# Optimization experiments

Hardware: AMD Instinct MI355X
Metric: run time of the kernel (lower is better)

## Reference

```python
import jax, jax.numpy as jnp
import numpy as np

B, D, H = 8, 14, 128          # trees, GCMN_DEPTH, HIDDEN_SIZE
N_LEAF = 2 ** (D - 1)          # leaves (= depth-1 nodes) per tree


def _build_tree():
    # level[d] = node ids at depth d within one tree
    level = [np.arange(N_LEAF, dtype=np.int32)]
    cur = N_LEAF
    for d in range(1, D + 1):
        cnt = N_LEAF >> (d - 1)
        level.append(np.arange(cur, cur + cnt, dtype=np.int32))
        cur += cnt
    npt = cur                                  # nodes per tree = 3n - 1
    offs = (np.arange(B, dtype=np.int32) * npt)[:, None]

    def batched(a):
        return (a[None, :] + offs).reshape(-1)

    src, dst, st = [], [], []
    # leaf block: depth-0 node -> its unique depth-1 node (edge_states = 0)
    src.append(batched(level[0]))
    dst.append(batched(level[1]))
    st.append(np.zeros(B * N_LEAF, np.float32))
    # depth d -> d+1 blocks: left children first, then right children
    for d in range(1, D):
        ch, pa = level[d], level[d + 1]
        left, right = ch[0::2], ch[1::2]
        src.append(np.concatenate([batched(left), batched(right)]))
        dst.append(np.concatenate([batched(pa), batched(pa)]))
        m = B * len(ch)
        st.append(np.concatenate([np.zeros(m // 2, np.float32), np.ones(m // 2, np.float32)]))
    return (np.concatenate(src), np.concatenate(dst), np.concatenate(st), B * npt)


def _dense(key, fin, fout):
    return jax.random.normal(key, (fin, fout), jnp.float32) / np.sqrt(fin)


def setup_inputs() -> dict:
    key = jax.random.key(0)
    esrc, edst, estates, n_nodes = _build_tree()
    ks = jax.random.split(key, 24)
    inp = {
        "x": jax.random.normal(ks[0], (n_nodes, H), jnp.float32),
        "edge_src": jnp.asarray(esrc),
        "edge_dst": jnp.asarray(edst),
        "edge_states": jnp.asarray(estates),
        "edge_features": jax.random.normal(ks[1], (B * N_LEAF, H), jnp.float32),
        "gcmn_depth": D,
    }
    specs = {"nem": 2 * H, "mg": 2 * H, "mr": H + 1}  # WideMLP input widths
    i = 2
    for name, fin in specs.items():
        dims = [(fin, H), (H, H), (H, H)]
        for j, (a, b) in enumerate(dims):
            inp[f"{name}_w{j}"] = _dense(ks[i], a, b); i += 1
            inp[f"{name}_b{j}"] = jnp.zeros((b,), jnp.float32)
    return inp


def _mlp3(h, w0, b0, w1, b1, w2, b2):
    # WideMLP(in, hidden, out, HIDDEN_LAYERS=2): two ReLU hidden layers + linear out
    h = jax.nn.relu(h @ w0 + b0)
    h = jax.nn.relu(h @ w1 + b1)
    return h @ w2 + b2


def reference(x, edge_src, edge_dst, edge_states, edge_features,
              nem_w0, nem_b0, nem_w1, nem_b1, nem_w2, nem_b2,
              mg_w0, mg_b0, mg_w1, mg_b1, mg_w2, mg_b2,
              mr_w0, mr_b0, mr_w1, mr_b1, mr_w2, mr_b2,
              gcmn_depth):
    Dn = int(gcmn_depth)
    nL = edge_features.shape[0]
    N = x.shape[0]
    # static offsets of the per-depth edge blocks (edges are depth-sorted)
    block_off = [0]
    off = nL
    for d in range(1, Dn):
        block_off.append(off)
        off += nL >> (d - 1)

    # ---- forward_up ----
    start_feat = x[edge_src[:nL]]                       # depth-0 node features
    merged = _mlp3(jnp.concatenate([start_feat, edge_features], axis=1),
                   nem_w0, nem_b0, nem_w1, nem_b1, nem_w2, nem_b2)
    x = x.at[edge_dst[:nL]].set(merged)                 # write depth-1 nodes
    for d in range(1, Dn):
        s = block_off[d]
        m = nL >> (d - 1)
        half = m // 2
        left = x[edge_src[s:s + half]]                  # edge_states == 0
        right = x[edge_src[s + half:s + m]]             # edge_states == 1
        par = edge_dst[s + half:s + m]
        x = x.at[par].set(_mlp3(jnp.concatenate([left, right], axis=1),
                                mg_w0, mg_b0, mg_w1, mg_b1, mg_w2, mg_b2))

    # ---- forward_down ----
    for depth in range(Dn, 0, -1):
        if depth == 1:
            s, m = 0, nL
        else:
            s = block_off[depth - 1]
            m = nL >> (depth - 2)
        src = edge_src[s:s + m]
        dst = edge_dst[s:s + m]
        st = edge_states[s:s + m]
        top = x[dst]
        bottom = x[src]
        merged = _mlp3(jnp.concatenate([top, st[:, None]], axis=1),
                       mr_w0, mr_b0, mr_w1, mr_b1, mr_w2, mr_b2)
        agg = jax.ops.segment_sum(merged, src, num_segments=N)  # scatter_sum
        x = x.at[src].set(agg[src] + bottom)
    return x
```

## Files before the change

### kernel.cpp

```cpp
#include <hip/hip_runtime.h>
#include <cstdint>
#include <cstddef>

typedef __attribute__((ext_vector_type(8))) short bf16x8;
typedef __attribute__((ext_vector_type(4))) float f32x4;

#define LO_OFF 184320

__device__ __forceinline__ unsigned short f2bf(float f) {
  union { float f; unsigned u; } c; c.f = f;
  unsigned u = c.u + 0x7fffu + ((c.u >> 16) & 1u);
  return (unsigned short)(u >> 16);
}
__device__ __forceinline__ float bf2f(unsigned short h) {
  union { unsigned u; float f; } c; c.u = ((unsigned)h) << 16;
  return c.f;
}

struct PrepP {
  const float* w[9];
  unsigned short* out;
};

__global__ __launch_bounds__(256) void prep_kernel(PrepP pp) {
  int gid = blockIdx.x * 256 + threadIdx.x;
  if (gid >= LO_OFF) return;
  const int Ks[9]  = {256,128,128, 256,128,128, 129,128,128};
  const int szs[9] = {32768,16384,16384, 32768,16384,16384, 20480,16384,16384};
  const int KCs[9] = {8,4,4, 8,4,4, 5,4,4};
  int m = 0, off = gid;
  while (m < 8 && off >= szs[m]) { off -= szs[m]; ++m; }
  int j    = off & 7;
  int t    = off >> 3;
  int lane = t & 63;
  int fc   = t >> 6;
  int KC   = KCs[m];
  int kc   = fc % KC;
  int nt   = fc / KC;
  int n = nt * 16 + (lane & 15);
  int k = kc * 32 + (lane >> 4) * 8 + j;
  float v = 0.f;
  if (k < Ks[m]) v = pp.w[m][(size_t)k * 128 + n];
  unsigned short hi = f2bf(v);
  unsigned short lo = f2bf(v - bf2f(hi));
  pp.out[gid] = hi;
  pp.out[LO_OFF + gid] = lo;
}

struct FP {
  const float* srcA;
  const float* srcB;
  const float* addbase;
  const int* esrc;
  const int* edst;
  const float* est;
  const unsigned short* w0;
  const unsigned short* w1;
  const unsigned short* w2;
  const float* b0;
  const float* b1;
  const float* b2;
  float* out;
  int s, half, rows;
};

template<int KC>
__device__ __forceinline__ void mfma_layer_to_h(
    char* AH, char* AL, int lane, int wrow0,
    const unsigned short* w, const float* bias) {
  bf16x8 ah[KC], al[KC];
  int arow = wrow0 + (lane & 15);
  int aswz = (arow & 7) << 4;
  #pragma unroll
  for (int kc = 0; kc < KC; ++kc) {
    int byt = (kc * 64 + (lane >> 4) * 16) ^ aswz;
    ah[kc] = *(const bf16x8*)(AH + arow * 512 + byt);
    al[kc] = *(const bf16x8*)(AL + arow * 512 + byt);
  }
  #pragma unroll
  for (int nt = 0; nt < 8; ++nt) {
    float bv = bias[nt * 16 + (lane & 15)];
    f32x4 acc = {bv, bv, bv, bv};
    #pragma unroll
    for (int kc = 0; kc < KC; ++kc) {
      const char* wb = (const char*)(w + (size_t)(nt * KC + kc) * 512) + lane * 16;
      bf16x8 bh = *(const bf16x8*)(wb);
      bf16x8 bl = *(const bf16x8*)(wb + (size_t)LO_OFF * 2);
      acc = __builtin_amdgcn_mfma_f32_16x16x32_bf16(ah[kc], bh, acc, 0, 0, 0);
      acc = __builtin_amdgcn_mfma_f32_16x16x32_bf16(ah[kc], bl, acc, 0, 0, 0);
      acc = __builtin_amdgcn_mfma_f32_16x16x32_bf16(al[kc], bh, acc, 0, 0, 0);
    }
    #pragma unroll
    for (int r = 0; r < 4; ++r) {
      float v = fmaxf(acc[r], 0.f);
      int row = wrow0 + (lane >> 4) * 4 + r;
      int cb = (nt * 32 + (lane & 15) * 2) ^ ((row & 7) << 4);
      unsigned short hv = f2bf(v);
      *(unsigned short*)(AH + row * 512 + cb) = hv;
      *(unsigned short*)(AL + row * 512 + cb) = f2bf(v - bf2f(hv));
    }
  }
}

__device__ __forceinline__ void stage_write(char* AH, char* AL, int row, int byt, float4 v) {
  unsigned short h0 = f2bf(v.x), h1 = f2bf(v.y), h2 = f2bf(v.z), h3 = f2bf(v.w);
  uint2 hw, lw;
  hw.x = (unsigned)h0 | ((unsigned)h1 << 16);
  hw.y = (unsigned)h2 | ((unsigned)h3 << 16);
  lw.x = (unsigned)f2bf(v.x - bf2f(h0)) | ((unsigned)f2bf(v.y - bf2f(h1)) << 16);
  lw.y = (unsigned)f2bf(v.z - bf2f(h2)) | ((unsigned)f2bf(v.w - bf2f(h3)) << 16);
  *(uint2*)(AH + row * 512 + byt) = hw;
  *(uint2*)(AL + row * 512 + byt) = lw;
}

template<int MODE>
__global__ __launch_bounds__(256) void fused_mlp(FP p) {
  __shared__ char AH[64 * 512];
  __shared__ char AL[64 * 512];
  const int tid = threadIdx.x;
  const int wid = tid >> 6;
  const int lane = tid & 63;
  const int tbase = blockIdx.x * 64;
  const int wrow0 = wid * 16;

  if (MODE != 2) {
    #pragma unroll
    for (int it = 0; it < 16; ++it) {
      int row = wrow0 + it;
      int rg = tbase + row;
      int f4 = lane;
      float4 v = {0.f, 0.f, 0.f, 0.f};
      if (rg < p.rows) {
        if (MODE == 0) {
          if (f4 < 32) { int node = p.esrc[rg]; v = *(const float4*)(p.srcA + (size_t)node * 128 + f4 * 4); }
          else         { v = *(const float4*)(p.srcB + (size_t)rg * 128 + (f4 - 32) * 4); }
        } else {
          if (f4 < 32) { int node = p.esrc[p.s + rg];          v = *(const float4*)(p.srcA + (size_t)node * 128 + f4 * 4); }
          else         { int node = p.esrc[p.s + p.half + rg]; v = *(const float4*)(p.srcA + (size_t)node * 128 + (f4 - 32) * 4); }
        }
      }
      int byt = (f4 * 8) ^ ((row & 7) << 4);
      stage_write(AH, AL, row, byt, v);
    }
  } else {
    #pragma unroll
    for (int it = 0; it < 8; ++it) {
      int li = it * 64 + lane;
      int rl = li >> 5;
      int f4 = li & 31;
      int row = wrow0 + rl;
      int rg = tbase + row;
      float4 v = {0.f, 0.f, 0.f, 0.f};
      if (rg < p.rows) { int node = p.edst[p.s + rg]; v = *(const float4*)(p.srcA + (size_t)node * 128 + f4 * 4); }
      int byt = (f4 * 8) ^ ((row & 7) << 4);
      stage_write(AH, AL, row, byt, v);
    }
    {
      int rl = lane >> 2;
      int ci = lane & 3;
      int row = wrow0 + rl;
      int rg = tbase + row;
      float sv = (rg < p.rows && ci == 0) ? p.est[p.s + rg] : 0.f;
      uint4 hz = {0u, 0u, 0u, 0u};
      uint4 lz = {0u, 0u, 0u, 0u};
      hz.x = (unsigned)f2bf(sv);
      int byt = (256 + ci * 16) ^ ((row & 7) << 4);
      *(uint4*)(AH + row * 512 + byt) = hz;
      *(uint4*)(AL + row * 512 + byt) = lz;
    }
  }
  __syncthreads();

  constexpr int KC0 = (MODE == 2) ? 5 : 8;
  mfma_layer_to_h<KC0>(AH, AL, lane, wrow0, p.w0, p.b0);
  __syncthreads();
  mfma_layer_to_h<4>(AH, AL, lane, wrow0, p.w1, p.b1);
  __syncthreads();

  {
    bf16x8 ah[4], al[4];
    int arow = wrow0 + (lane & 15);
    int aswz = (arow & 7) << 4;
    #pragma unroll
    for (int kc = 0; kc < 4; ++kc) {
      int byt = (kc * 64 + (lane >> 4) * 16) ^ aswz;
      ah[kc] = *(const bf16x8*)(AH + arow * 512 + byt);
      al[kc] = *(const bf16x8*)(AL + arow * 512 + byt);
    }
    int nodes[4]; bool vld[4];
    #pragma unroll
    for (int r = 0; r < 4; ++r) {
      int rg = tbase + wrow0 + (lane >> 4) * 4 + r;
      vld[r] = rg < p.rows;
      int e = 0;
      if (vld[r]) {
        if (MODE == 0)      e = p.edst[rg];
        else if (MODE == 1) e = p.edst[p.s + rg];
        else                e = p.esrc[p.s + rg];
      }
      nodes[r] = e;
    }
    #pragma unroll
    for (int nt = 0; nt < 8; ++nt) {
      float bv = p.b2[nt * 16 + (lane & 15)];
      f32x4 acc = {bv, bv, bv, bv};
      #pragma unroll
      for (int kc = 0; kc < 4; ++kc) {
        const char* wb = (const char*)(p.w2 + (size_t)(nt * 4 + kc) * 512) + lane * 16;
        bf16x8 bh = *(const bf16x8*)(wb);
        bf16x8 bl = *(const bf16x8*)(wb + (size_t)LO_OFF * 2);
        acc = __builtin_amdgcn_mfma_f32_16x16x32_bf16(ah[kc], bh, acc, 0, 0, 0);
        acc = __builtin_amdgcn_mfma_f32_16x16x32_bf16(ah[kc], bl, acc, 0, 0, 0);
        acc = __builtin_amdgcn_mfma_f32_16x16x32_bf16(al[kc], bh, acc, 0, 0, 0);
      }
      int col = nt * 16 + (lane & 15);
      #pragma unroll
      for (int r = 0; r < 4; ++r) {
        if (vld[r]) {
          float v = acc[r];
          if (MODE == 2) v += p.addbase[(size_t)nodes[r] * 128 + col];
          p.out[(size_t)nodes[r] * 128 + col] = v;
        }
      }
    }
  }
}

extern "C" void kernel_launch(void* const* d_in, const int* in_sizes, int n_in,
                              void* d_out, int out_size, void* d_ws, size_t ws_size,
                              hipStream_t stream) {
  const float* xin  = (const float*)d_in[0];
  const int*   esrc = (const int*)d_in[1];
  const int*   edst = (const int*)d_in[2];
  const float* est  = (const float*)d_in[3];
  const float* ef   = (const float*)d_in[4];
  unsigned short* wsb = (unsigned short*)d_ws;
  float* xw = (float*)d_out;

  PrepP pp;
  const int widx[9] = {6, 8, 10, 12, 14, 16, 18, 20, 22};
  for (int i = 0; i < 9; ++i) pp.w[i] = (const float*)d_in[widx[i]];
  pp.out = wsb;
  prep_kernel<<<dim3(720), dim3(256), 0, stream>>>(pp);

  int blk[14], off[14];
  blk[0] = 65536; off[0] = 0;
  for (int d = 1; d <= 13; ++d) { blk[d] = 65536 >> (d - 1); off[d] = off[d - 1] + blk[d - 1]; }

  auto fill = [&](FP& p, int s, int half, int rows, const float* addb,
                  int w0o, int w1o, int w2o, int b0i, int b1i, int b2i) {
    p.addbase = addb;
    p.esrc = esrc; p.edst = edst; p.est = est;
    p.w0 = wsb + w0o; p.w1 = wsb + w1o; p.w2 = wsb + w2o;
    p.b0 = (const float*)d_in[b0i]; p.b1 = (const float*)d_in[b1i]; p.b2 = (const float*)d_in[b2i];
    p.out = xw;
    p.s = s; p.half = half; p.rows = rows;
  };

  {
    FP p; p.srcA = xin; p.srcB = ef;
    fill(p, 0, 0, 65536, nullptr, 0, 32768, 49152, 7, 9, 11);
    fused_mlp<0><<<dim3(1024), dim3(256), 0, stream>>>(p);
  }
  for (int d = 1; d <= 13; ++d) {
    FP p; p.srcA = xw; p.srcB = xw;
    int rows = blk[d] / 2;
    fill(p, off[d], rows, rows, nullptr, 65536, 98304, 114688, 13, 15, 17);
    fused_mlp<1><<<dim3((rows + 63) / 64), dim3(256), 0, stream>>>(p);
  }
  for (int bi = 13; bi >= 0; --bi) {
    FP p; p.srcA = xw; p.srcB = xw;
    int rows = blk[bi];
    const float* addb = (bi == 0) ? xin : xw;
    fill(p, off[bi], 0, rows, addb, 131072, 151552, 167936, 19, 21, 23);
    fused_mlp<2><<<dim3((rows + 63) / 64), dim3(256), 0, stream>>>(p);
  }
}
```

Baseline: 1.036 ms.

## Fuse small tree levels into persistent kernel with grid barriers; shrink tiles to 16 rows

The small levels (up-pass depths 5-13 and down-pass levels 13-6) now run inside one persistent 128-block kernel that separates levels with an atomic-counter grid barrier, replacing many tiny launches. Tiles shrink from 64 to 16 rows per block, and the 4 waves split the output columns instead of the rows, which gives more blocks for the small levels and a smaller shared-memory footprint. The goal is to remove per-launch overhead and tail underutilisation on the serial level chain. In exchange, each block rereads weights for only 16 rows, the large levels get more blocks, and the spin barrier adds latency and depends on all 128 blocks being resident at once.

```diff
diff --git a/kernel.cpp b/kernel.cpp
--- a/kernel.cpp
+++ b/kernel.cpp
@@ -4,22 +4,31 @@
 
 typedef __attribute__((ext_vector_type(8))) short bf16x8;
 typedef __attribute__((ext_vector_type(4))) float f32x4;
+typedef unsigned short u16;
 
 #define LO_OFF 184320
-
-__device__ __forceinline__ unsigned short f2bf(float f) {
+#define MFMA16(a,b,c) __builtin_amdgcn_mfma_f32_16x16x32_bf16((a),(b),(c),0,0,0)
+
+__device__ __forceinline__ u16 f2bf(float f) {
   union { float f; unsigned u; } c; c.f = f;
   unsigned u = c.u + 0x7fffu + ((c.u >> 16) & 1u);
-  return (unsigned short)(u >> 16);
-}
-__device__ __forceinline__ float bf2f(unsigned short h) {
+  return (u16)(u >> 16);
+}
+__device__ __forceinline__ float bf2f(u16 h) {
   union { unsigned u; float f; } c; c.u = ((unsigned)h) << 16;
   return c.f;
 }
+__device__ __forceinline__ void split4(float4 v, uint2& hw, uint2& lw) {
+  u16 h0 = f2bf(v.x), h1 = f2bf(v.y), h2 = f2bf(v.z), h3 = f2bf(v.w);
+  hw.x = (unsigned)h0 | ((unsigned)h1 << 16);
+  hw.y = (unsigned)h2 | ((unsigned)h3 << 16);
+  lw.x = (unsigned)f2bf(v.x - bf2f(h0)) | ((unsigned)f2bf(v.y - bf2f(h1)) << 16);
+  lw.y = (unsigned)f2bf(v.z - bf2f(h2)) | ((unsigned)f2bf(v.w - bf2f(h3)) << 16);
+}
 
 struct PrepP {
   const float* w[9];
-  unsigned short* out;
+  u16* out;
 };
 
 __global__ __launch_bounds__(256) void prep_kernel(PrepP pp) {
@@ -41,188 +50,225 @@
   int k = kc * 32 + (lane >> 4) * 8 + j;
   float v = 0.f;
   if (k < Ks[m]) v = pp.w[m][(size_t)k * 128 + n];
-  unsigned short hi = f2bf(v);
-  unsigned short lo = f2bf(v - bf2f(hi));
+  u16 hi = f2bf(v);
+  u16 lo = f2bf(v - bf2f(hi));
   pp.out[gid] = hi;
   pp.out[LO_OFF + gid] = lo;
 }
 
-struct FP {
-  const float* srcA;
-  const float* srcB;
-  const float* addbase;
-  const int* esrc;
-  const int* edst;
-  const float* est;
-  const unsigned short* w0;
-  const unsigned short* w1;
-  const unsigned short* w2;
-  const float* b0;
-  const float* b1;
-  const float* b2;
+struct LP {
+  const float* srcA; const float* srcB; const float* addb;
+  const int* esrc; const int* edst; const float* est;
+  const u16 *w0, *w1, *w2;
+  const float *b0, *b1, *b2;
   float* out;
   int s, half, rows;
 };
 
-template<int KC>
-__device__ __forceinline__ void mfma_layer_to_h(
-    char* AH, char* AL, int lane, int wrow0,
-    const unsigned short* w, const float* bias) {
-  bf16x8 ah[KC], al[KC];
-  int arow = wrow0 + (lane & 15);
-  int aswz = (arow & 7) << 4;
+template<int KC, int LDA>
+__device__ __forceinline__ void layer_mid(const u16* AH, const u16* AL, u16* OH, u16* OL,
+                                          int lane, int wv, const u16* wgt, const float* bias) {
+  const int arow = lane & 15;
+  const int g = lane >> 4;
+  const int aswz = (arow & 7) << 4;
+  const char* ahb = (const char*)AH + arow * LDA;
+  const char* alb = (const char*)AL + arow * LDA;
+  const int nt0 = wv * 2;
+  float bv0 = bias[nt0 * 16 + arow];
+  float bv1 = bias[nt0 * 16 + 16 + arow];
+  f32x4 acc0 = {bv0, bv0, bv0, bv0};
+  f32x4 acc1 = {bv1, bv1, bv1, bv1};
   #pragma unroll
   for (int kc = 0; kc < KC; ++kc) {
-    int byt = (kc * 64 + (lane >> 4) * 16) ^ aswz;
-    ah[kc] = *(const bf16x8*)(AH + arow * 512 + byt);
-    al[kc] = *(const bf16x8*)(AL + arow * 512 + byt);
-  }
-  #pragma unroll
-  for (int nt = 0; nt < 8; ++nt) {
-    float bv = bias[nt * 16 + (lane & 15)];
-    f32x4 acc = {bv, bv, bv, bv};
-    #pragma unroll
-    for (int kc = 0; kc < KC; ++kc) {
-      const char* wb = (const char*)(w + (size_t)(nt * KC + kc) * 512) + lane * 16;
-      bf16x8 bh = *(const bf16x8*)(wb);
-      bf16x8 bl = *(const bf16x8*)(wb + (size_t)LO_OFF * 2);
-      acc = __builtin_amdgcn_mfma_f32_16x16x32_bf16(ah[kc], bh, acc, 0, 0, 0);
-      acc = __builtin_amdgcn_mfma_f32_16x16x32_bf16(ah[kc], bl, acc, 0, 0, 0);
-      acc = __builtin_amdgcn_mfma_f32_16x16x32_bf16(al[kc], bh, acc, 0, 0, 0);
+    int byt = (kc * 64 + g * 16) ^ aswz;
+    bf16x8 ah = *(const bf16x8*)(ahb + byt);
+    bf16x8 al = *(const bf16x8*)(alb + byt);
+    const u16* wb0 = wgt + (size_t)(nt0 * KC + kc) * 512 + lane * 8;
+    const u16* wb1 = wb0 + (size_t)KC * 512;
+    bf16x8 bh0 = *(const bf16x8*)wb0;
+    bf16x8 bl0 = *(const bf16x8*)(wb0 + LO_OFF);
+    bf16x8 bh1 = *(const bf16x8*)wb1;
+    bf16x8 bl1 = *(const bf16x8*)(wb1 + LO_OFF);
+    acc0 = MFMA16(ah, bh0, acc0); acc1 = MFMA16(ah, bh1, acc1);
+    acc0 = MFMA16(ah, bl0, acc0); acc1 = MFMA16(ah, bl1, acc1);
+    acc0 = MFMA16(al, bh0, acc0); acc1 = MFMA16(al, bh1, acc1);
+  }
+  #pragma unroll
+  for (int r = 0; r < 4; ++r) {
+    int row = g * 4 + r;
+    int oswz = (row & 7) << 4;
+    char* oh = (char*)OH + row * 256;
+    char* ol = (char*)OL + row * 256;
+    float v0 = fmaxf(acc0[r], 0.f);
+    float v1 = fmaxf(acc1[r], 0.f);
+    int c0 = ((nt0 * 16 + arow) * 2) ^ oswz;
+    int c1 = ((nt0 * 16 + 16 + arow) * 2) ^ oswz;
+    u16 h0 = f2bf(v0), h1 = f2bf(v1);
+    *(u16*)(oh + c0) = h0; *(u16*)(ol + c0) = f2bf(v0 - bf2f(h0));
+    *(u16*)(oh + c1) = h1; *(u16*)(ol + c1) = f2bf(v1 - bf2f(h1));
+  }
+}
+
+template<int MODE>
+__device__ __forceinline__ void layer_out(const u16* AH, const u16* AL,
+                                          int lane, int wv, const LP& p, int tbase) {
+  const int arow = lane & 15;
+  const int g = lane >> 4;
+  const int aswz = (arow & 7) << 4;
+  const char* ahb = (const char*)AH + arow * 256;
+  const char* alb = (const char*)AL + arow * 256;
+  const int nt0 = wv * 2;
+  float bv0 = p.b2[nt0 * 16 + arow];
+  float bv1 = p.b2[nt0 * 16 + 16 + arow];
+  f32x4 acc0 = {bv0, bv0, bv0, bv0};
+  f32x4 acc1 = {bv1, bv1, bv1, bv1};
+
+  int nodes[4]; bool vld[4];
+  #pragma unroll
+  for (int r = 0; r < 4; ++r) {
+    int rg = tbase + g * 4 + r;
+    vld[r] = rg < p.rows;
+    int e = 0;
+    if (vld[r]) e = (MODE == 2) ? p.esrc[p.s + rg]
+                 : ((MODE == 0) ? p.edst[rg] : p.edst[p.s + rg]);
+    nodes[r] = e;
+  }
+  #pragma unroll
+  for (int kc = 0; kc < 4; ++kc) {
+    int byt = (kc * 64 + g * 16) ^ aswz;
+    bf16x8 ah = *(const bf16x8*)(ahb + byt);
+    bf16x8 al = *(const bf16x8*)(alb + byt);
+    const u16* wb0 = p.w2 + (size_t)(nt0 * 4 + kc) * 512 + lane * 8;
+    const u16* wb1 = wb0 + (size_t)4 * 512;
+    bf16x8 bh0 = *(const bf16x8*)wb0;
+    bf16x8 bl0 = *(const bf16x8*)(wb0 + LO_OFF);
+    bf16x8 bh1 = *(const bf16x8*)wb1;
+    bf16x8 bl1 = *(const bf16x8*)(wb1 + LO_OFF);
+    acc0 = MFMA16(ah, bh0, acc0); acc1 = MFMA16(ah, bh1, acc1);
+    acc0 = MFMA16(ah, bl0, acc0); acc1 = MFMA16(ah, bl1, acc1);
+    acc0 = MFMA16(al, bh0, acc0); acc1 = MFMA16(al, bh1, acc1);
+  }
+  int col0 = nt0 * 16 + arow, col1 = col0 + 16;
+  #pragma unroll
+  for (int r = 0; r < 4; ++r) {
+    if (vld[r]) {
+      float v0 = acc0[r], v1 = acc1[r];
+      size_t b = (size_t)nodes[r] * 128;
+      if (MODE == 2) { v0 += p.addb[b + col0]; v1 += p.addb[b + col1]; }
+      p.out[b + col0] = v0;
+      p.out[b + col1] = v1;
     }
-    #pragma unroll
-    for (int r = 0; r < 4; ++r) {
-      float v = fmaxf(acc[r], 0.f);
-      int row = wrow0 + (lane >> 4) * 4 + r;
-      int cb = (nt * 32 + (lane & 15) * 2) ^ ((row & 7) << 4);
-      unsigned short hv = f2bf(v);
-      *(unsigned short*)(AH + row * 512 + cb) = hv;
-      *(unsigned short*)(AL + row * 512 + cb) = f2bf(v - bf2f(hv));
+  }
+}
+
+template<int MODE>
+__device__ __forceinline__ void mlp_tile(u16* SH, u16* SL, u16* HH, u16* HL,
+                                         const LP& p, int tbase) {
+  const int tid = threadIdx.x;
+  const int lane = tid & 63;
+  const int wv = tid >> 6;
+  {
+    int row = tid >> 4, q = tid & 15;
+    int rg = tbase + row;
+    int swz = (row & 7) << 4;
+    char* sh = (char*)SH + row * 512;
+    char* sl = (char*)SL + row * 512;
+    bool ok = rg < p.rows;
+    if (MODE != 2) {
+      const float* pL = nullptr; const float* pR = nullptr;
+      if (ok) {
+        if (MODE == 0) { pL = p.srcA + (size_t)p.esrc[rg] * 128; pR = p.srcB + (size_t)rg * 128; }
+        else           { pL = p.srcA + (size_t)p.esrc[p.s + rg] * 128;
+                         pR = p.srcA + (size_t)p.esrc[p.s + p.half + rg] * 128; }
+      }
+      #pragma unroll
+      for (int i = 0; i < 4; ++i) {
+        int f4 = q * 4 + i;
+        float4 v = {0.f, 0.f, 0.f, 0.f};
+        if (ok) v = (f4 < 32) ? *(const float4*)(pL + f4 * 4) : *(const float4*)(pR + (f4 - 32) * 4);
+        uint2 hw, lw; split4(v, hw, lw);
+        int byt = (f4 * 8) ^ swz;
+        *(uint2*)(sh + byt) = hw; *(uint2*)(sl + byt) = lw;
+      }
+    } else {
+      const float* pT = ok ? p.srcA + (size_t)p.edst[p.s + rg] * 128 : nullptr;
+      #pragma unroll
+      for (int i = 0; i < 2; ++i) {
+        int f4 = q * 2 + i;
+        float4 v = {0.f, 0.f, 0.f, 0.f};
+        if (ok) v = *(const float4*)(pT + f4 * 4);
+        uint2 hw, lw; split4(v, hw, lw);
+        int byt = (f4 * 8) ^ swz;
+        *(uint2*)(sh + byt) = hw; *(uint2*)(sl + byt) = lw;
+      }
+      if (q < 4) {
+        float sv = (q == 0 && ok) ? p.est[p.s + rg] : 0.f;
+        uint4 hz = {0u, 0u, 0u, 0u}, lz = {0u, 0u, 0u, 0u};
+        hz.x = (unsigned)f2bf(sv);
+        int byt = (256 + q * 16) ^ swz;
+        *(uint4*)(sh + byt) = hz;
+        *(uint4*)(sl + byt) = lz;
+      }
     }
   }
-}
-
-__device__ __forceinline__ void stage_write(char* AH, char* AL, int row, int byt, float4 v) {
-  unsigned short h0 = f2bf(v.x), h1 = f2bf(v.y), h2 = f2bf(v.z), h3 = f2bf(v.w);
-  uint2 hw, lw;
-  hw.x = (unsigned)h0 | ((unsigned)h1 << 16);
-  hw.y = (unsigned)h2 | ((unsigned)h3 << 16);
-  lw.x = (unsigned)f2bf(v.x - bf2f(h0)) | ((unsigned)f2bf(v.y - bf2f(h1)) << 16);
-  lw.y = (unsigned)f2bf(v.z - bf2f(h2)) | ((unsigned)f2bf(v.w - bf2f(h3)) << 16);
-  *(uint2*)(AH + row * 512 + byt) = hw;
-  *(uint2*)(AL + row * 512 + byt) = lw;
+  __syncthreads();
+  layer_mid<(MODE == 2 ? 5 : 8), 512>(SH, SL, HH, HL, lane, wv, p.w0, p.b0);
+  __syncthreads();
+  layer_mid<4, 256>(HH, HL, SH, SL, lane, wv, p.w1, p.b1);
+  __syncthreads();
+  layer_out<MODE>(SH, SL, lane, wv, p, tbase);
 }
 
 template<int MODE>
-__global__ __launch_bounds__(256) void fused_mlp(FP p) {
-  __shared__ char AH[64 * 512];
-  __shared__ char AL[64 * 512];
-  const int tid = threadIdx.x;
-  const int wid = tid >> 6;
-  const int lane = tid & 63;
-  const int tbase = blockIdx.x * 64;
-  const int wrow0 = wid * 16;
-
-  if (MODE != 2) {
-    #pragma unroll
-    for (int it = 0; it < 16; ++it) {
-      int row = wrow0 + it;
-      int rg = tbase + row;
-      int f4 = lane;
-      float4 v = {0.f, 0.f, 0.f, 0.f};
-      if (rg < p.rows) {
-        if (MODE == 0) {
-          if (f4 < 32) { int node = p.esrc[rg]; v = *(const float4*)(p.srcA + (size_t)node * 128 + f4 * 4); }
-          else         { v = *(const float4*)(p.srcB + (size_t)rg * 128 + (f4 - 32) * 4); }
-        } else {
-          if (f4 < 32) { int node = p.esrc[p.s + rg];          v = *(const float4*)(p.srcA + (size_t)node * 128 + f4 * 4); }
-          else         { int node = p.esrc[p.s + p.half + rg]; v = *(const float4*)(p.srcA + (size_t)node * 128 + (f4 - 32) * 4); }
-        }
-      }
-      int byt = (f4 * 8) ^ ((row & 7) << 4);
-      stage_write(AH, AL, row, byt, v);
+__global__ __launch_bounds__(256) void level_kernel(LP p) {
+  __shared__ u16 SH[16 * 256];
+  __shared__ u16 SL[16 * 256];
+  __shared__ u16 HH[16 * 128];
+  __shared__ u16 HL[16 * 128];
+  mlp_tile<MODE>(SH, SL, HH, HL, p, blockIdx.x * 16);
+}
+
+struct GP {
+  const int* esrc; const int* edst; const float* est;
+  float* xw;
+  const u16 *gw0, *gw1, *gw2; const float *gb0, *gb1, *gb2;
+  const u16 *rw0, *rw1, *rw2; const float *rb0, *rb1, *rb2;
+  unsigned* cnt;
+  int nlev;
+  int mode[17]; int s[17]; int rows[17];
+};
+
+__global__ __launch_bounds__(256) void fused_kernel(GP g) {
+  __shared__ u16 SH[16 * 256];
+  __shared__ u16 SL[16 * 256];
+  __shared__ u16 HH[16 * 128];
+  __shared__ u16 HL[16 * 128];
+  const unsigned nb = gridDim.x;
+  for (int li = 0; li < g.nlev; ++li) {
+    int rows = g.rows[li];
+    int tbase = blockIdx.x * 16;
+    if (tbase < rows) {
+      LP p;
+      p.esrc = g.esrc; p.edst = g.edst; p.est = g.est;
+      p.srcA = g.xw; p.srcB = g.xw; p.addb = g.xw; p.out = g.xw;
+      p.s = g.s[li]; p.half = rows; p.rows = rows;
+      if (g.mode[li] == 1) {
+        p.w0 = g.gw0; p.w1 = g.gw1; p.w2 = g.gw2; p.b0 = g.gb0; p.b1 = g.gb1; p.b2 = g.gb2;
+        mlp_tile<1>(SH, SL, HH, HL, p, tbase);
+      } else {
+        p.w0 = g.rw0; p.w1 = g.rw1; p.w2 = g.rw2; p.b0 = g.rb0; p.b1 = g.rb1; p.b2 = g.rb2;
+        mlp_tile<2>(SH, SL, HH, HL, p, tbase);
+      }
     }
-  } else {
-    #pragma unroll
-    for (int it = 0; it < 8; ++it) {
-      int li = it * 64 + lane;
-      int rl = li >> 5;
-      int f4 = li & 31;
-      int row = wrow0 + rl;
-      int rg = tbase + row;
-      float4 v = {0.f, 0.f, 0.f, 0.f};
-      if (rg < p.rows) { int node = p.edst[p.s + rg]; v = *(const float4*)(p.srcA + (size_t)node * 128 + f4 * 4); }
-      int byt = (f4 * 8) ^ ((row & 7) << 4);
-      stage_write(AH, AL, row, byt, v);
+    __syncthreads();
+    if (threadIdx.x == 0) {
+      __threadfence();
+      __hip_atomic_fetch_add(g.cnt + li, 1u, __ATOMIC_ACQ_REL, __HIP_MEMORY_SCOPE_AGENT);
+      while (__hip_atomic_load(g.cnt + li, __ATOMIC_ACQUIRE, __HIP_MEMORY_SCOPE_AGENT) < nb) {
+        __builtin_amdgcn_s_sleep(2);
+      }
     }
-    {
-      int rl = lane >> 2;
-      int ci = lane & 3;
-      int row = wrow0 + rl;
-      int rg = tbase + row;
-      float sv = (rg < p.rows && ci == 0) ? p.est[p.s + rg] : 0.f;
-      uint4 hz = {0u, 0u, 0u, 0u};
-      uint4 lz = {0u, 0u, 0u, 0u};
-      hz.x = (unsigned)f2bf(sv);
-      int byt = (256 + ci * 16) ^ ((row & 7) << 4);
-      *(uint4*)(AH + row * 512 + byt) = hz;
-      *(uint4*)(AL + row * 512 + byt) = lz;
-    }
-  }
-  __syncthreads();
-
-  constexpr int KC0 = (MODE == 2) ? 5 : 8;
-  mfma_layer_to_h<KC0>(AH, AL, lane, wrow0, p.w0, p.b0);
-  __syncthreads();
-  mfma_layer_to_h<4>(AH, AL, lane, wrow0, p.w1, p.b1);
-  __syncthreads();
-
-  {
-    bf16x8 ah[4], al[4];
-    int arow = wrow0 + (lane & 15);
-    int aswz = (arow & 7) << 4;
-    #pragma unroll
-    for (int kc = 0; kc < 4; ++kc) {
-      int byt = (kc * 64 + (lane >> 4) * 16) ^ aswz;
-      ah[kc] = *(const bf16x8*)(AH + arow * 512 + byt);
-      al[kc] = *(const bf16x8*)(AL + arow * 512 + byt);
-    }
-    int nodes[4]; bool vld[4];
-    #pragma unroll
-    for (int r = 0; r < 4; ++r) {
-      int rg = tbase + wrow0 + (lane >> 4) * 4 + r;
-      vld[r] = rg < p.rows;
-      int e = 0;
-      if (vld[r]) {
-        if (MODE == 0)      e = p.edst[rg];
-        else if (MODE == 1) e = p.edst[p.s + rg];
-        else                e = p.esrc[p.s + rg];
-      }
-      nodes[r] = e;
-    }
-    #pragma unroll
-    for (int nt = 0; nt < 8; ++nt) {
-      float bv = p.b2[nt * 16 + (lane & 15)];
-      f32x4 acc = {bv, bv, bv, bv};
-      #pragma unroll
-      for (int kc = 0; kc < 4; ++kc) {
-        const char* wb = (const char*)(p.w2 + (size_t)(nt * 4 + kc) * 512) + lane * 16;
-        bf16x8 bh = *(const bf16x8*)(wb);
-        bf16x8 bl = *(const bf16x8*)(wb + (size_t)LO_OFF * 2);
-        acc = __builtin_amdgcn_mfma_f32_16x16x32_bf16(ah[kc], bh, acc, 0, 0, 0);
-        acc = __builtin_amdgcn_mfma_f32_16x16x32_bf16(ah[kc], bl, acc, 0, 0, 0);
-        acc = __builtin_amdgcn_mfma_f32_16x16x32_bf16(al[kc], bh, acc, 0, 0, 0);
-      }
-      int col = nt * 16 + (lane & 15);
-      #pragma unroll
-      for (int r = 0; r < 4; ++r) {
-        if (vld[r]) {
-          float v = acc[r];
-          if (MODE == 2) v += p.addbase[(size_t)nodes[r] * 128 + col];
-          p.out[(size_t)nodes[r] * 128 + col] = v;
-        }
-      }
-    }
+    __syncthreads();
   }
 }
 
@@ -234,45 +280,62 @@
   const int*   edst = (const int*)d_in[2];
   const float* est  = (const float*)d_in[3];
   const float* ef   = (const float*)d_in[4];
-  unsigned short* wsb = (unsigned short*)d_ws;
+  u16* wsb = (u16*)d_ws;
   float* xw = (float*)d_out;
+  unsigned* cnt = (unsigned*)((char*)d_ws + 737280);
 
   PrepP pp;
   const int widx[9] = {6, 8, 10, 12, 14, 16, 18, 20, 22};
   for (int i = 0; i < 9; ++i) pp.w[i] = (const float*)d_in[widx[i]];
   pp.out = wsb;
   prep_kernel<<<dim3(720), dim3(256), 0, stream>>>(pp);
+  hipMemsetAsync(cnt, 0, 128, stream);
 
   int blk[14], off[14];
   blk[0] = 65536; off[0] = 0;
   for (int d = 1; d <= 13; ++d) { blk[d] = 65536 >> (d - 1); off[d] = off[d - 1] + blk[d - 1]; }
 
-  auto fill = [&](FP& p, int s, int half, int rows, const float* addb,
-                  int w0o, int w1o, int w2o, int b0i, int b1i, int b2i) {
-    p.addbase = addb;
-    p.esrc = esrc; p.edst = edst; p.est = est;
-    p.w0 = wsb + w0o; p.w1 = wsb + w1o; p.w2 = wsb + w2o;
-    p.b0 = (const float*)d_in[b0i]; p.b1 = (const float*)d_in[b1i]; p.b2 = (const float*)d_in[b2i];
-    p.out = xw;
-    p.s = s; p.half = half; p.rows = rows;
+  auto base = [&](LP& p) {
+    p.esrc = esrc; p.edst = edst; p.est = est; p.out = xw;
+    p.srcA = xw; p.srcB = xw; p.addb = xw;
   };
 
   {
-    FP p; p.srcA = xin; p.srcB = ef;
-    fill(p, 0, 0, 65536, nullptr, 0, 32768, 49152, 7, 9, 11);
-    fused_mlp<0><<<dim3(1024), dim3(256), 0, stream>>>(p);
-  }
-  for (int d = 1; d <= 13; ++d) {
-    FP p; p.srcA = xw; p.srcB = xw;
+    LP p; base(p);
+    p.srcA = xin; p.srcB = ef;
+    p.w0 = wsb + 0; p.w1 = wsb + 32768; p.w2 = wsb + 49152;
+    p.b0 = (const float*)d_in[7]; p.b1 = (const float*)d_in[9]; p.b2 = (const float*)d_in[11];
+    p.s = 0; p.half = 0; p.rows = 65536;
+    level_kernel<0><<<dim3(4096), dim3(256), 0, stream>>>(p);
+  }
+  for (int d = 1; d <= 4; ++d) {
+    LP p; base(p);
     int rows = blk[d] / 2;
-    fill(p, off[d], rows, rows, nullptr, 65536, 98304, 114688, 13, 15, 17);
-    fused_mlp<1><<<dim3((rows + 63) / 64), dim3(256), 0, stream>>>(p);
-  }
-  for (int bi = 13; bi >= 0; --bi) {
-    FP p; p.srcA = xw; p.srcB = xw;
+    p.w0 = wsb + 65536; p.w1 = wsb + 98304; p.w2 = wsb + 114688;
+    p.b0 = (const float*)d_in[13]; p.b1 = (const float*)d_in[15]; p.b2 = (const float*)d_in[17];
+    p.s = off[d]; p.half = rows; p.rows = rows;
+    level_kernel<1><<<dim3((rows + 15) / 16), dim3(256), 0, stream>>>(p);
+  }
+  {
+    GP g;
+    g.esrc = esrc; g.edst = edst; g.est = est; g.xw = xw; g.cnt = cnt;
+    g.gw0 = wsb + 65536; g.gw1 = wsb + 98304; g.gw2 = wsb + 114688;
+    g.gb0 = (const float*)d_in[13]; g.gb1 = (const float*)d_in[15]; g.gb2 = (const float*)d_in[17];
+    g.rw0 = wsb + 131072; g.rw1 = wsb + 151552; g.rw2 = wsb + 167936;
+    g.rb0 = (const float*)d_in[19]; g.rb1 = (const float*)d_in[21]; g.rb2 = (const float*)d_in[23];
+    int li = 0;
+    for (int d = 5; d <= 13; ++d) { g.mode[li] = 1; g.s[li] = off[d]; g.rows[li] = blk[d] / 2; ++li; }
+    for (int bi = 13; bi >= 6; --bi) { g.mode[li] = 2; g.s[li] = off[bi]; g.rows[li] = blk[bi]; ++li; }
+    g.nlev = li;
+    fused_kernel<<<dim3(128), dim3(256), 0, stream>>>(g);
+  }
+  for (int bi = 5; bi >= 0; --bi) {
+    LP p; base(p);
     int rows = blk[bi];
-    const float* addb = (bi == 0) ? xin : xw;
-    fill(p, off[bi], 0, rows, addb, 131072, 151552, 167936, 19, 21, 23);
-    fused_mlp<2><<<dim3((rows + 63) / 64), dim3(256), 0, stream>>>(p);
-  }
-}
+    p.addb = (bi == 0) ? xin : xw;
+    p.w0 = wsb + 131072; p.w1 = wsb + 151552; p.w2 = wsb + 167936;
+    p.b0 = (const float*)d_in[19]; p.b1 = (const float*)d_in[21]; p.b2 = (const float*)d_in[23];
+    p.s = off[bi]; p.half = 0; p.rows = rows;
+    level_kernel<2><<<dim3((rows + 15) / 16), dim3(256), 0, stream>>>(p);
+  }
+}
```

Result: faster. 982.3 us (-5.1%).

## Fuse small tree levels into one per-tree kernel and use per-wave tiles

Applied to the files above, without the earlier changes.

Levels 5–13 of the up pass and 13–6 of the down pass now run in one persistent kernel with one block per tree, synchronising levels with block barriers instead of separate kernel launches. The MLP tile is restructured so each wave owns its 16-row LDS tile, staging inputs in 128-column halves and keeping accumulators in registers, so there are no block-wide barriers. LDS drops to 32KB with launch_bounds(256,3) for higher occupancy. The fused kernel uses only 8 blocks, so parallelism on those levels is limited, and correctness depends on nodes of different trees never mixing, which the per-tree indexing assumes.

```diff
diff --git a/kernel.cpp b/kernel.cpp
--- a/kernel.cpp
+++ b/kernel.cpp
@@ -3,23 +3,37 @@
 #include <cstddef>
 
 typedef __attribute__((ext_vector_type(8))) short bf16x8;
+typedef bf16x8 __attribute__((may_alias)) bf16x8_a;
 typedef __attribute__((ext_vector_type(4))) float f32x4;
+typedef unsigned short u16;
+typedef u16 __attribute__((may_alias)) u16_a;
+typedef uint2 __attribute__((may_alias)) uint2_a;
+typedef uint4 __attribute__((may_alias)) uint4_a;
 
 #define LO_OFF 184320
-
-__device__ __forceinline__ unsigned short f2bf(float f) {
+#define MFMA16(a,b,c) __builtin_amdgcn_mfma_f32_16x16x32_bf16((a),(b),(c),0,0,0)
+#define LDS_FENCE() asm volatile("" ::: "memory")
+
+__device__ __forceinline__ u16 f2bf(float f) {
   union { float f; unsigned u; } c; c.f = f;
   unsigned u = c.u + 0x7fffu + ((c.u >> 16) & 1u);
-  return (unsigned short)(u >> 16);
-}
-__device__ __forceinline__ float bf2f(unsigned short h) {
+  return (u16)(u >> 16);
+}
+__device__ __forceinline__ float bf2f(u16 h) {
   union { unsigned u; float f; } c; c.u = ((unsigned)h) << 16;
   return c.f;
 }
+__device__ __forceinline__ void split4(float4 v, uint2& hw, uint2& lw) {
+  u16 h0 = f2bf(v.x), h1 = f2bf(v.y), h2 = f2bf(v.z), h3 = f2bf(v.w);
+  hw.x = (unsigned)h0 | ((unsigned)h1 << 16);
+  hw.y = (unsigned)h2 | ((unsigned)h3 << 16);
+  lw.x = (unsigned)f2bf(v.x - bf2f(h0)) | ((unsigned)f2bf(v.y - bf2f(h1)) << 16);
+  lw.y = (unsigned)f2bf(v.z - bf2f(h2)) | ((unsigned)f2bf(v.w - bf2f(h3)) << 16);
+}
 
 struct PrepP {
   const float* w[9];
-  unsigned short* out;
+  u16* out;
 };
 
 __global__ __launch_bounds__(256) void prep_kernel(PrepP pp) {
@@ -41,188 +55,228 @@
   int k = kc * 32 + (lane >> 4) * 8 + j;
   float v = 0.f;
   if (k < Ks[m]) v = pp.w[m][(size_t)k * 128 + n];
-  unsigned short hi = f2bf(v);
-  unsigned short lo = f2bf(v - bf2f(hi));
+  u16 hi = f2bf(v);
+  u16 lo = f2bf(v - bf2f(hi));
   pp.out[gid] = hi;
   pp.out[LO_OFF + gid] = lo;
 }
 
-struct FP {
-  const float* srcA;
-  const float* srcB;
-  const float* addbase;
-  const int* esrc;
-  const int* edst;
-  const float* est;
-  const unsigned short* w0;
-  const unsigned short* w1;
-  const unsigned short* w2;
-  const float* b0;
-  const float* b1;
-  const float* b2;
+struct WTP {
+  const float* gA;
+  const float* gB;
+  const float* addb;
+  const int* esrc; const int* edst; const float* est;
+  const u16 *w0, *w1, *w2;
+  const float *b0, *b1, *b2;
   float* out;
-  int s, half, rows;
+  int s, half;
 };
 
-template<int KC>
-__device__ __forceinline__ void mfma_layer_to_h(
-    char* AH, char* AL, int lane, int wrow0,
-    const unsigned short* w, const float* bias) {
-  bf16x8 ah[KC], al[KC];
-  int arow = wrow0 + (lane & 15);
-  int aswz = (arow & 7) << 4;
+template<int MODE>
+__device__ __forceinline__ void wave_tile(const WTP& p, char* SH, char* SL, int lane,
+                                          int base1, int base2, int split, int nvalid) {
+  const int g = lane >> 4;
+  const int q = lane & 15;
+  const int aswz = (q & 7) << 4;
+
+  auto eidx = [&](int r) {
+    int rc = (r < nvalid) ? r : 0;
+    if (MODE == 2) return (rc < split) ? (base1 + rc) : (base2 + (rc - split));
+    return base1 + rc;
+  };
+
+  bf16x8 ah[4], al[4];
+  f32x4 acc[8];
+
+  auto initacc = [&](const float* b) {
+    #pragma unroll
+    for (int nt = 0; nt < 8; ++nt) { float bv = b[nt * 16 + q]; acc[nt] = (f32x4){bv, bv, bv, bv}; }
+  };
+
+  auto stage128 = [&](int c) {
+    int rl = lane >> 5;
+    int f4 = lane & 31;
+    #pragma unroll
+    for (int i = 0; i < 8; ++i) {
+      int row = i * 2 + rl;
+      int e = eidx(row);
+      const float* src;
+      if (MODE == 0)      src = (c == 0) ? p.gA + (size_t)p.esrc[e] * 128
+                                         : p.gB + (size_t)e * 128;
+      else if (MODE == 1) src = p.gA + (size_t)p.esrc[p.s + (c ? p.half + e : e)] * 128;
+      else                src = p.gA + (size_t)p.edst[p.s + e] * 128;
+      float4 v = *(const float4*)(src + f4 * 4);
+      uint2 hw, lw; split4(v, hw, lw);
+      int byt = (f4 * 8) ^ ((row & 7) << 4);
+      *(uint2_a*)(SH + row * 256 + byt) = hw;
+      *(uint2_a*)(SL + row * 256 + byt) = lw;
+    }
+  };
+
+  auto frags = [&](int nkc) {
+    #pragma unroll
+    for (int kc = 0; kc < 4; ++kc) {
+      if (kc < nkc) {
+        int byt = (kc * 64 + g * 16) ^ aswz;
+        ah[kc] = *(const bf16x8_a*)(SH + q * 256 + byt);
+        al[kc] = *(const bf16x8_a*)(SL + q * 256 + byt);
+      }
+    }
+  };
+
+  auto accum = [&](const u16* whi, int kcb, int nkc, int KCw) {
+    const u16* wlo = whi + LO_OFF;
+    #pragma unroll
+    for (int nt = 0; nt < 8; ++nt) {
+      #pragma unroll
+      for (int kc = 0; kc < 4; ++kc) {
+        if (kc < nkc) {
+          size_t o = ((size_t)(nt * KCw + kcb + kc) << 9) + lane * 8;
+          bf16x8 bh = *(const bf16x8*)(whi + o);
+          bf16x8 bl = *(const bf16x8*)(wlo + o);
+          acc[nt] = MFMA16(ah[kc], bh, acc[nt]);
+          acc[nt] = MFMA16(ah[kc], bl, acc[nt]);
+          acc[nt] = MFMA16(al[kc], bh, acc[nt]);
+        }
+      }
+    }
+  };
+
+  auto writeH = [&]() {
+    #pragma unroll
+    for (int nt = 0; nt < 8; ++nt) {
+      int col = nt * 16 + q;
+      #pragma unroll
+      for (int r = 0; r < 4; ++r) {
+        int row = g * 4 + r;
+        float v = fmaxf(acc[nt][r], 0.f);
+        int byt = (col * 2) ^ ((row & 7) << 4);
+        u16 hv = f2bf(v);
+        *(u16_a*)(SH + row * 256 + byt) = hv;
+        *(u16_a*)(SL + row * 256 + byt) = f2bf(v - bf2f(hv));
+      }
+    }
+  };
+
+  initacc(p.b0);
+  stage128(0);
+  LDS_FENCE();
+  frags(4);
+  if (MODE != 2) {
+    accum(p.w0, 0, 4, 8);
+    LDS_FENCE();
+    stage128(1);
+    LDS_FENCE();
+    frags(4);
+    accum(p.w0, 4, 4, 8);
+  } else {
+    accum(p.w0, 0, 4, 5);
+    LDS_FENCE();
+    {
+      int row = lane >> 2, c4 = lane & 3;
+      float sv = (c4 == 0) ? p.est[p.s + eidx(row)] : 0.f;
+      uint4 hz = {0u, 0u, 0u, 0u}, lz = {0u, 0u, 0u, 0u};
+      hz.x = (unsigned)f2bf(sv);
+      int byt = (c4 * 16) ^ ((row & 7) << 4);
+      *(uint4_a*)(SH + row * 256 + byt) = hz;
+      *(uint4_a*)(SL + row * 256 + byt) = lz;
+    }
+    LDS_FENCE();
+    frags(1);
+    accum(p.w0, 4, 1, 5);
+  }
+  LDS_FENCE();
+  writeH();
+  LDS_FENCE();
+
+  initacc(p.b1);
+  frags(4);
+  accum(p.w1, 0, 4, 4);
+  LDS_FENCE();
+  writeH();
+  LDS_FENCE();
+
+  initacc(p.b2);
+  frags(4);
+  accum(p.w2, 0, 4, 4);
+  int nodes[4];
   #pragma unroll
-  for (int kc = 0; kc < KC; ++kc) {
-    int byt = (kc * 64 + (lane >> 4) * 16) ^ aswz;
-    ah[kc] = *(const bf16x8*)(AH + arow * 512 + byt);
-    al[kc] = *(const bf16x8*)(AL + arow * 512 + byt);
+  for (int r = 0; r < 4; ++r) {
+    int rr = g * 4 + r;
+    bool v = rr < nvalid;
+    int e = eidx(rr);
+    int nd = -1;
+    if (v) nd = (MODE == 0) ? p.edst[e] : ((MODE == 1) ? p.edst[p.s + e] : p.esrc[p.s + e]);
+    nodes[r] = nd;
   }
   #pragma unroll
   for (int nt = 0; nt < 8; ++nt) {
-    float bv = bias[nt * 16 + (lane & 15)];
-    f32x4 acc = {bv, bv, bv, bv};
-    #pragma unroll
-    for (int kc = 0; kc < KC; ++kc) {
-      const char* wb = (const char*)(w + (size_t)(nt * KC + kc) * 512) + lane * 16;
-      bf16x8 bh = *(const bf16x8*)(wb);
-      bf16x8 bl = *(const bf16x8*)(wb + (size_t)LO_OFF * 2);
-      acc = __builtin_amdgcn_mfma_f32_16x16x32_bf16(ah[kc], bh, acc, 0, 0, 0);
-      acc = __builtin_amdgcn_mfma_f32_16x16x32_bf16(ah[kc], bl, acc, 0, 0, 0);
-      acc = __builtin_amdgcn_mfma_f32_16x16x32_bf16(al[kc], bh, acc, 0, 0, 0);
-    }
+    int col = nt * 16 + q;
     #pragma unroll
     for (int r = 0; r < 4; ++r) {
-      float v = fmaxf(acc[r], 0.f);
-      int row = wrow0 + (lane >> 4) * 4 + r;
-      int cb = (nt * 32 + (lane & 15) * 2) ^ ((row & 7) << 4);
-      unsigned short hv = f2bf(v);
-      *(unsigned short*)(AH + row * 512 + cb) = hv;
-      *(unsigned short*)(AL + row * 512 + cb) = f2bf(v - bf2f(hv));
-    }
-  }
-}
-
-__device__ __forceinline__ void stage_write(char* AH, char* AL, int row, int byt, float4 v) {
-  unsigned short h0 = f2bf(v.x), h1 = f2bf(v.y), h2 = f2bf(v.z), h3 = f2bf(v.w);
-  uint2 hw, lw;
-  hw.x = (unsigned)h0 | ((unsigned)h1 << 16);
-  hw.y = (unsigned)h2 | ((unsigned)h3 << 16);
-  lw.x = (unsigned)f2bf(v.x - bf2f(h0)) | ((unsigned)f2bf(v.y - bf2f(h1)) << 16);
-  lw.y = (unsigned)f2bf(v.z - bf2f(h2)) | ((unsigned)f2bf(v.w - bf2f(h3)) << 16);
-  *(uint2*)(AH + row * 512 + byt) = hw;
-  *(uint2*)(AL + row * 512 + byt) = lw;
+      if (nodes[r] >= 0) {
+        float v = acc[nt][r];
+        if (MODE == 2) v += p.addb[(size_t)nodes[r] * 128 + col];
+        p.out[(size_t)nodes[r] * 128 + col] = v;
+      }
+    }
+  }
 }
 
 template<int MODE>
-__global__ __launch_bounds__(256) void fused_mlp(FP p) {
-  __shared__ char AH[64 * 512];
-  __shared__ char AL[64 * 512];
-  const int tid = threadIdx.x;
-  const int wid = tid >> 6;
-  const int lane = tid & 63;
-  const int tbase = blockIdx.x * 64;
-  const int wrow0 = wid * 16;
-
-  if (MODE != 2) {
-    #pragma unroll
-    for (int it = 0; it < 16; ++it) {
-      int row = wrow0 + it;
-      int rg = tbase + row;
-      int f4 = lane;
-      float4 v = {0.f, 0.f, 0.f, 0.f};
-      if (rg < p.rows) {
-        if (MODE == 0) {
-          if (f4 < 32) { int node = p.esrc[rg]; v = *(const float4*)(p.srcA + (size_t)node * 128 + f4 * 4); }
-          else         { v = *(const float4*)(p.srcB + (size_t)rg * 128 + (f4 - 32) * 4); }
-        } else {
-          if (f4 < 32) { int node = p.esrc[p.s + rg];          v = *(const float4*)(p.srcA + (size_t)node * 128 + f4 * 4); }
-          else         { int node = p.esrc[p.s + p.half + rg]; v = *(const float4*)(p.srcA + (size_t)node * 128 + (f4 - 32) * 4); }
-        }
-      }
-      int byt = (f4 * 8) ^ ((row & 7) << 4);
-      stage_write(AH, AL, row, byt, v);
-    }
-  } else {
-    #pragma unroll
-    for (int it = 0; it < 8; ++it) {
-      int li = it * 64 + lane;
-      int rl = li >> 5;
-      int f4 = li & 31;
-      int row = wrow0 + rl;
-      int rg = tbase + row;
-      float4 v = {0.f, 0.f, 0.f, 0.f};
-      if (rg < p.rows) { int node = p.edst[p.s + rg]; v = *(const float4*)(p.srcA + (size_t)node * 128 + f4 * 4); }
-      int byt = (f4 * 8) ^ ((row & 7) << 4);
-      stage_write(AH, AL, row, byt, v);
-    }
-    {
-      int rl = lane >> 2;
-      int ci = lane & 3;
-      int row = wrow0 + rl;
-      int rg = tbase + row;
-      float sv = (rg < p.rows && ci == 0) ? p.est[p.s + rg] : 0.f;
-      uint4 hz = {0u, 0u, 0u, 0u};
-      uint4 lz = {0u, 0u, 0u, 0u};
-      hz.x = (unsigned)f2bf(sv);
-      int byt = (256 + ci * 16) ^ ((row & 7) << 4);
-      *(uint4*)(AH + row * 512 + byt) = hz;
-      *(uint4*)(AL + row * 512 + byt) = lz;
-    }
-  }
-  __syncthreads();
-
-  constexpr int KC0 = (MODE == 2) ? 5 : 8;
-  mfma_layer_to_h<KC0>(AH, AL, lane, wrow0, p.w0, p.b0);
-  __syncthreads();
-  mfma_layer_to_h<4>(AH, AL, lane, wrow0, p.w1, p.b1);
-  __syncthreads();
-
-  {
-    bf16x8 ah[4], al[4];
-    int arow = wrow0 + (lane & 15);
-    int aswz = (arow & 7) << 4;
-    #pragma unroll
-    for (int kc = 0; kc < 4; ++kc) {
-      int byt = (kc * 64 + (lane >> 4) * 16) ^ aswz;
-      ah[kc] = *(const bf16x8*)(AH + arow * 512 + byt);
-      al[kc] = *(const bf16x8*)(AL + arow * 512 + byt);
-    }
-    int nodes[4]; bool vld[4];
-    #pragma unroll
-    for (int r = 0; r < 4; ++r) {
-      int rg = tbase + wrow0 + (lane >> 4) * 4 + r;
-      vld[r] = rg < p.rows;
-      int e = 0;
-      if (vld[r]) {
-        if (MODE == 0)      e = p.edst[rg];
-        else if (MODE == 1) e = p.edst[p.s + rg];
-        else                e = p.esrc[p.s + rg];
-      }
-      nodes[r] = e;
-    }
-    #pragma unroll
-    for (int nt = 0; nt < 8; ++nt) {
-      float bv = p.b2[nt * 16 + (lane & 15)];
-      f32x4 acc = {bv, bv, bv, bv};
-      #pragma unroll
-      for (int kc = 0; kc < 4; ++kc) {
-        const char* wb = (const char*)(p.w2 + (size_t)(nt * 4 + kc) * 512) + lane * 16;
-        bf16x8 bh = *(const bf16x8*)(wb);
-        bf16x8 bl = *(const bf16x8*)(wb + (size_t)LO_OFF * 2);
-        acc = __builtin_amdgcn_mfma_f32_16x16x32_bf16(ah[kc], bh, acc, 0, 0, 0);
-        acc = __builtin_amdgcn_mfma_f32_16x16x32_bf16(ah[kc], bl, acc, 0, 0, 0);
-        acc = __builtin_amdgcn_mfma_f32_16x16x32_bf16(al[kc], bh, acc, 0, 0, 0);
-      }
-      int col = nt * 16 + (lane & 15);
-      #pragma unroll
-      for (int r = 0; r < 4; ++r) {
-        if (vld[r]) {
-          float v = acc[r];
-          if (MODE == 2) v += p.addbase[(size_t)nodes[r] * 128 + col];
-          p.out[(size_t)nodes[r] * 128 + col] = v;
-        }
-      }
-    }
+__global__ __launch_bounds__(256, 3) void level_kernel(WTP p, int rows) {
+  __shared__ char LB[32768];
+  int wv = threadIdx.x >> 6, lane = threadIdx.x & 63;
+  char* SH = LB + wv * 8192;
+  char* SL = SH + 4096;
+  int t16 = (blockIdx.x * 4 + wv) * 16;
+  if (t16 >= rows) return;
+  int nv = rows - t16; if (nv > 16) nv = 16;
+  wave_tile<MODE>(p, SH, SL, lane, t16, 0, 16, nv);
+}
+
+struct FGP {
+  WTP g;
+  WTP r;
+  int nlev;
+  int mode[17], s[17], half[17], m[17];
+};
+
+__global__ __launch_bounds__(256, 3) void tiny_fused(FGP fp) {
+  __shared__ char LB[32768];
+  int wv = threadIdx.x >> 6, lane = threadIdx.x & 63;
+  char* SH = LB + wv * 8192;
+  char* SL = SH + 4096;
+  int b = blockIdx.x;
+  for (int li = 0; li < fp.nlev; ++li) {
+    if (fp.mode[li] == 1) {
+      int half = fp.half[li];
+      int rt = half >> 3;
+      int tiles = (rt + 15) >> 4;
+      WTP p = fp.g; p.s = fp.s[li]; p.half = half;
+      for (int t = wv; t < tiles; t += 4) {
+        int r0 = t * 16;
+        int nv = rt - r0; if (nv > 16) nv = 16;
+        wave_tile<1>(p, SH, SL, lane, b * rt + r0, 0, 16, nv);
+      }
+    } else {
+      int m = fp.m[li];
+      int hs = m >> 4;
+      int rt = m >> 3;
+      int tiles = (rt + 15) >> 4;
+      WTP p = fp.r; p.s = fp.s[li]; p.half = 0;
+      for (int t = wv; t < tiles; t += 4) {
+        int r0 = t * 16;
+        int nv = rt - r0; if (nv > 16) nv = 16;
+        int b1, b2, sp;
+        if (r0 + 16 <= hs)      { b1 = b * hs + r0;                     b2 = 0; sp = 16; }
+        else if (r0 >= hs)      { b1 = (m >> 1) + b * hs + (r0 - hs);   b2 = 0; sp = 16; }
+        else                    { b1 = b * hs + r0; b2 = (m >> 1) + b * hs; sp = hs - r0; }
+        wave_tile<2>(p, SH, SL, lane, b1, b2, sp, nv);
+      }
+    }
+    __threadfence_block();
+    __syncthreads();
   }
 }
 
@@ -234,7 +288,7 @@
   const int*   edst = (const int*)d_in[2];
   const float* est  = (const float*)d_in[3];
   const float* ef   = (const float*)d_in[4];
-  unsigned short* wsb = (unsigned short*)d_ws;
+  u16* wsb = (u16*)d_ws;
   float* xw = (float*)d_out;
 
   PrepP pp;
@@ -247,32 +301,45 @@
   blk[0] = 65536; off[0] = 0;
   for (int d = 1; d <= 13; ++d) { blk[d] = 65536 >> (d - 1); off[d] = off[d - 1] + blk[d - 1]; }
 
-  auto fill = [&](FP& p, int s, int half, int rows, const float* addb,
-                  int w0o, int w1o, int w2o, int b0i, int b1i, int b2i) {
-    p.addbase = addb;
-    p.esrc = esrc; p.edst = edst; p.est = est;
-    p.w0 = wsb + w0o; p.w1 = wsb + w1o; p.w2 = wsb + w2o;
-    p.b0 = (const float*)d_in[b0i]; p.b1 = (const float*)d_in[b1i]; p.b2 = (const float*)d_in[b2i];
-    p.out = xw;
-    p.s = s; p.half = half; p.rows = rows;
-  };
+  WTP nem;
+  nem.gA = xin; nem.gB = ef; nem.addb = nullptr;
+  nem.esrc = esrc; nem.edst = edst; nem.est = est;
+  nem.w0 = wsb + 0; nem.w1 = wsb + 32768; nem.w2 = wsb + 49152;
+  nem.b0 = (const float*)d_in[7]; nem.b1 = (const float*)d_in[9]; nem.b2 = (const float*)d_in[11];
+  nem.out = xw; nem.s = 0; nem.half = 0;
+
+  WTP mg = nem;
+  mg.gA = xw; mg.gB = nullptr;
+  mg.w0 = wsb + 65536; mg.w1 = wsb + 98304; mg.w2 = wsb + 114688;
+  mg.b0 = (const float*)d_in[13]; mg.b1 = (const float*)d_in[15]; mg.b2 = (const float*)d_in[17];
+
+  WTP mr = nem;
+  mr.gA = xw; mr.addb = xw;
+  mr.w0 = wsb + 131072; mr.w1 = wsb + 151552; mr.w2 = wsb + 167936;
+  mr.b0 = (const float*)d_in[19]; mr.b1 = (const float*)d_in[21]; mr.b2 = (const float*)d_in[23];
+
+  level_kernel<0><<<dim3(1024), dim3(256), 0, stream>>>(nem, 65536);
+
+  for (int d = 1; d <= 4; ++d) {
+    int rows = blk[d] / 2;
+    WTP p = mg; p.s = off[d]; p.half = rows;
+    level_kernel<1><<<dim3((rows + 63) / 64), dim3(256), 0, stream>>>(p, rows);
+  }
 
   {
-    FP p; p.srcA = xin; p.srcB = ef;
-    fill(p, 0, 0, 65536, nullptr, 0, 32768, 49152, 7, 9, 11);
-    fused_mlp<0><<<dim3(1024), dim3(256), 0, stream>>>(p);
-  }
-  for (int d = 1; d <= 13; ++d) {
-    FP p; p.srcA = xw; p.srcB = xw;
-    int rows = blk[d] / 2;
-    fill(p, off[d], rows, rows, nullptr, 65536, 98304, 114688, 13, 15, 17);
-    fused_mlp<1><<<dim3((rows + 63) / 64), dim3(256), 0, stream>>>(p);
-  }
-  for (int bi = 13; bi >= 0; --bi) {
-    FP p; p.srcA = xw; p.srcB = xw;
+    FGP fp;
+    fp.g = mg; fp.r = mr;
+    int li = 0;
+    for (int d = 5; d <= 13; ++d) { fp.mode[li] = 1; fp.s[li] = off[d]; fp.half[li] = blk[d] / 2; fp.m[li] = 0; ++li; }
+    for (int bi = 13; bi >= 6; --bi) { fp.mode[li] = 2; fp.s[li] = off[bi]; fp.half[li] = 0; fp.m[li] = blk[bi]; ++li; }
+    fp.nlev = li;
+    tiny_fused<<<dim3(8), dim3(256), 0, stream>>>(fp);
+  }
+
+  for (int bi = 5; bi >= 0; --bi) {
     int rows = blk[bi];
-    const float* addb = (bi == 0) ? xin : xw;
-    fill(p, off[bi], 0, rows, addb, 131072, 151552, 167936, 19, 21, 23);
-    fused_mlp<2><<<dim3((rows + 63) / 64), dim3(256), 0, stream>>>(p);
-  }
-}
+    WTP p = mr; p.s = off[bi];
+    p.addb = (bi == 0) ? xin : xw;
+    level_kernel<2><<<dim3((rows + 63) / 64), dim3(256), 0, stream>>>(p, rows);
+  }
+}
```

New measurement: 2.214 ms. 114% more time.
